# Kernel optimization log

Measured on AMD Instinct MI355X. Metric: run time of the kernel, lower is better.

## Reference

```python
import jax, jax.numpy as jnp
import numpy as np
import math

EMBED_DIM = 1024
NUM_HEADS = 16
HEAD_DIM = EMBED_DIM // NUM_HEADS
SEQ = 1024
BATCH = 8


def setup_inputs() -> dict:
    key = jax.random.key(0)
    k1, k2, k3, k4, k5 = jax.random.split(key, 5)
    q = jax.random.normal(k1, (SEQ, BATCH, EMBED_DIM), dtype=jnp.float32)
    # module asserts key == query (self-attention only)
    in_proj_w = jax.random.normal(k2, (3 * EMBED_DIM, EMBED_DIM), dtype=jnp.float32) * 0.02
    in_proj_b = jax.random.normal(k3, (3 * EMBED_DIM,), dtype=jnp.float32) * 0.02
    out_proj_w = jax.random.normal(k4, (EMBED_DIM, EMBED_DIM), dtype=jnp.float32) * 0.02
    out_proj_b = jax.random.normal(k5, (EMBED_DIM,), dtype=jnp.float32) * 0.02
    return {
        "query": q,
        "key": q,
        "value": q,
        "in_proj_w": in_proj_w,
        "in_proj_b": in_proj_b,
        "out_proj_w": out_proj_w,
        "out_proj_b": out_proj_b,
    }


def reference(query, key, value, in_proj_w, in_proj_b, out_proj_w, out_proj_b):
    s, b, e = query.shape
    nh, hd = NUM_HEADS, HEAD_DIM
    norm = math.sqrt(hd)
    # fused QKV projection: [s, b, 3e]
    mixed = query @ in_proj_w.T + in_proj_b
    mixed = mixed.reshape(s, b, nh, 3 * hd)
    q, k, v = jnp.split(mixed, 3, axis=-1)  # each [s, b, nh, hd]
    # -> [b*nh, s, hd]
    q = q.reshape(s, b * nh, hd).transpose(1, 0, 2) / norm
    k = k.reshape(s, b * nh, hd).transpose(1, 0, 2)
    v = v.reshape(s, b * nh, hd).transpose(1, 0, 2)
    # full O(s^2) attention matrix, as in the original bmm/softmax/bmm
    scores = jnp.einsum('nqd,nkd->nqk', q, k)  # [b*nh, s, s]
    probs = jax.nn.softmax(scores, axis=-1)
    ctx = jnp.einsum('nqk,nkd->nqd', probs, v)  # [b*nh, s, hd]
    # [b*nh, s, hd] -> [s, b, e]
    ctx = ctx.reshape(b, nh, s, hd).transpose(2, 0, 1, 3).reshape(s, b, e)
    return ctx @ out_proj_w.T + out_proj_b
```

## Files before the change

### kernel.cpp

```cpp
#include <hip/hip_runtime.h>

typedef __bf16 bf16_t;
typedef __bf16 bf16x4 __attribute__((ext_vector_type(4)));
typedef __bf16 bf16x8 __attribute__((ext_vector_type(8)));
typedef float f32x4 __attribute__((ext_vector_type(4)));

#define MFMA16(a, b, c) __builtin_amdgcn_mfma_f32_16x16x32_bf16((a), (b), (c), 0, 0, 0)

__device__ __forceinline__ const bf16_t* tile_ptr(const bf16_t* t, int row, int kchunk) {
    return t + row * 64 + (((kchunk ^ (row & 7))) << 3);
}

__device__ __forceinline__ void stage64(const bf16_t* __restrict__ gbase, size_t gstride,
                                        bf16_t* lds_rowbase, int lane) {
    const int rr = lane >> 3, cl = lane & 7;
    const bf16_t* g = gbase + (size_t)rr * gstride + ((cl ^ rr) << 3);
    __builtin_amdgcn_global_load_lds((__attribute__((address_space(1))) const void*)g,
                                     (__attribute__((address_space(3))) void*)lds_rowbase,
                                     16, 0, 0);
}

__device__ __forceinline__ int cs_addr(int m, int n) {
    return m * 128 + ((((n >> 3) ^ ((m >> 3) & 7))) << 3) + (n & 7);
}

__global__ void __launch_bounds__(256) k_cvt(
    const float* __restrict__ q, const float* __restrict__ wi, const float* __restrict__ wo,
    bf16_t* __restrict__ qb, bf16_t* __restrict__ wib, bf16_t* __restrict__ wob)
{
    const int g = blockIdx.x * 256 + threadIdx.x;
    const float* src; bf16_t* dst; int off;
    if (g < 1048576)      { src = q;  dst = qb;  off = g; }
    else if (g < 1441792) { src = wi; dst = wib; off = g - 1048576; }
    else                  { src = wo; dst = wob; off = g - 1441792; }
    const float4* s4 = (const float4*)(src + (size_t)off * 8);
    float4 a = s4[0], b = s4[1];
    bf16x8 v;
    v[0] = (bf16_t)a.x; v[1] = (bf16_t)a.y; v[2] = (bf16_t)a.z; v[3] = (bf16_t)a.w;
    v[4] = (bf16_t)b.x; v[5] = (bf16_t)b.y; v[6] = (bf16_t)b.z; v[7] = (bf16_t)b.w;
    *(bf16x8*)(dst + (size_t)off * 8) = v;
}

__global__ void __launch_bounds__(256) k_qkv(
    const bf16_t* __restrict__ A, const bf16_t* __restrict__ W,
    const float* __restrict__ bias,
    bf16_t* __restrict__ Qh, bf16_t* __restrict__ Kh, bf16_t* __restrict__ Vt)
{
    __shared__ bf16_t smem[16384];
    bf16_t* As = smem;
    bf16_t* Bs = smem + 8192;
    const int m0 = blockIdx.x * 128;
    const int n0 = blockIdx.y * 128;
    const int which = n0 >> 10;
    const int hbase = (n0 & 1023) >> 6;
    const int t = threadIdx.x;
    const int wave = t >> 6, lane = t & 63;
    const int quad = lane >> 4, l16 = lane & 15;
    const int wm = (wave & 1) * 64, wn = (wave >> 1) * 64;

    f32x4 acc[4][4] = {};

    for (int k0 = 0; k0 < 1024; k0 += 64) {
        __syncthreads();
        #pragma unroll
        for (int p = 0; p < 4; ++p) {
            const int rb = wave * 32 + p * 8;
            stage64(A + (size_t)(m0 + rb) * 1024 + k0, 1024, As + rb * 64, lane);
            const int np = n0 + rb;
            const int wrow = ((np & 1023) >> 6) * 192 + which * 64 + (np & 63);
            stage64(W + (size_t)wrow * 1024 + k0, 1024, Bs + rb * 64, lane);
        }
        __syncthreads();
        #pragma unroll
        for (int ks = 0; ks < 2; ++ks) {
            bf16x8 af[4], bf[4];
            #pragma unroll
            for (int i = 0; i < 4; ++i)
                af[i] = *(const bf16x8*)tile_ptr(As, wm + i * 16 + l16, ks * 4 + quad);
            #pragma unroll
            for (int j = 0; j < 4; ++j)
                bf[j] = *(const bf16x8*)tile_ptr(Bs, wn + j * 16 + l16, ks * 4 + quad);
            #pragma unroll
            for (int i = 0; i < 4; ++i)
                #pragma unroll
                for (int j = 0; j < 4; ++j)
                    acc[i][j] = MFMA16(af[i], bf[j], acc[i][j]);
        }
    }

    __syncthreads();
    const float scale = (which == 0) ? 0.180336880111112f : 1.0f;
    #pragma unroll
    for (int j = 0; j < 4; ++j) {
        const int nl = wn + j * 16 + l16;
        const float bv = bias[(hbase + (nl >> 6)) * 192 + which * 64 + (nl & 63)];
        #pragma unroll
        for (int i = 0; i < 4; ++i) {
            #pragma unroll
            for (int rg = 0; rg < 4; ++rg) {
                const int ml = wm + i * 16 + quad * 4 + rg;
                smem[cs_addr(ml, nl)] = (bf16_t)((acc[i][j][rg] + bv) * scale);
            }
        }
    }
    __syncthreads();

    const int si0 = m0 >> 3;
    if (which < 2) {
        bf16_t* dst = which ? Kh : Qh;
        #pragma unroll
        for (int u = 0; u < 4; ++u) {
            const int unit = wave * 4 + u;
            const int h = unit >> 3, bi = unit & 7;
            const int head = bi * 16 + hbase + h;
            #pragma unroll
            for (int pass = 0; pass < 2; ++pass) {
                const int si = pass * 8 + (lane >> 3);
                const int dc = lane & 7;
                const int ml = si * 8 + bi;
                const int nch = (h * 8 + dc) ^ (si & 7);
                bf16x8 v = *(const bf16x8*)&smem[ml * 128 + nch * 8];
                *(bf16x8*)(dst + (size_t)head * 65536 + (size_t)(si0 + si) * 64 + dc * 8) = v;
            }
        }
    } else {
        #pragma unroll
        for (int u = 0; u < 8; ++u) {
            const int unit = wave * 8 + u;
            const int h = unit >> 4, bi = (unit >> 1) & 7, c = unit & 1;
            const int head = bi * 16 + hbase + h;
            const int d = lane;
            bf16x8 v;
            #pragma unroll
            for (int e = 0; e < 8; ++e) {
                const int ml = (c * 8 + e) * 8 + bi;
                const int nch = (h * 8 + (d >> 3)) ^ e;
                v[e] = smem[ml * 128 + nch * 8 + (d & 7)];
            }
            *(bf16x8*)(Vt + (size_t)head * 65536 +
                       (size_t)(si0 / 8 + c) * 512 + (size_t)d * 8) = v;
        }
    }
}

__global__ void __launch_bounds__(256, 4) k_attn(
    const bf16_t* __restrict__ Qh, const bf16_t* __restrict__ Kh,
    const bf16_t* __restrict__ Vg, bf16_t* __restrict__ Ctx)
{
    __shared__ bf16_t Ks[64 * 64];
    __shared__ bf16_t Vts[64 * 64];
    __shared__ bf16_t Pw[4][32 * 64];

    const int bid = blockIdx.x;
    const int head = (bid & 7) * 16 + ((bid >> 3) & 15);
    const int qt = bid >> 7;
    const int t = threadIdx.x;
    const int wave = t >> 6, lane = t & 63;
    const int quad = lane >> 4, l16 = lane & 15;

    const bf16_t* Qg = Qh + (size_t)head * 65536 + (size_t)qt * 8192;
    const bf16_t* Kg = Kh + (size_t)head * 65536;
    const bf16_t* Vgh = Vg + (size_t)head * 65536;

    bf16x8 qf[2][2];
    #pragma unroll
    for (int half = 0; half < 2; ++half)
        #pragma unroll
        for (int ks = 0; ks < 2; ++ks)
            qf[half][ks] = *(const bf16x8*)(
                Qg + (size_t)(wave * 32 + half * 16 + l16) * 64 + ks * 32 + quad * 8);

    bf16x8 ones;
    #pragma unroll
    for (int e = 0; e < 8; ++e) ones[e] = (bf16_t)((l16 == 0) ? 1.0f : 0.0f);

    f32x4 vacc[2][5] = {};

    for (int kt = 0; kt < 16; ++kt) {
        __syncthreads();
        #pragma unroll
        for (int p = 0; p < 2; ++p) {
            const int rb = wave * 16 + p * 8;
            stage64(Kg + (size_t)(kt * 64 + rb) * 64, 64, Ks + rb * 64, lane);
            {
                const int rr = lane >> 3, cl = lane & 7;
                const bf16_t* g = Vgh + (size_t)(kt * 8 + (cl ^ rr)) * 512
                                      + (size_t)(rb + rr) * 8;
                __builtin_amdgcn_global_load_lds(
                    (__attribute__((address_space(1))) const void*)g,
                    (__attribute__((address_space(3))) void*)(Vts + rb * 64), 16, 0, 0);
            }
        }
        __syncthreads();

        f32x4 s[2][4] = {};
        #pragma unroll
        for (int ks = 0; ks < 2; ++ks) {
            #pragma unroll
            for (int j = 0; j < 4; ++j) {
                bf16x8 kf = *(const bf16x8*)tile_ptr(Ks, j * 16 + l16, ks * 4 + quad);
                s[0][j] = MFMA16(kf, qf[0][ks], s[0][j]);
                s[1][j] = MFMA16(kf, qf[1][ks], s[1][j]);
            }
        }

        #pragma unroll
        for (int half = 0; half < 2; ++half) {
            const int row = half * 16 + l16;
            #pragma unroll
            for (int j = 0; j < 4; ++j) {
                bf16x4 pv;
                #pragma unroll
                for (int rg = 0; rg < 4; ++rg)
                    pv[rg] = (bf16_t)exp2f(s[half][j][rg]);
                const int chunk = j * 2 + (quad >> 1);
                *(bf16x4*)&Pw[wave][row * 64 + ((chunk ^ (row & 7)) << 3) + (quad & 1) * 4] = pv;
            }
        }
        asm volatile("s_waitcnt lgkmcnt(0)" ::: "memory");

        #pragma unroll
        for (int ks = 0; ks < 2; ++ks) {
            bf16x8 pf0 = *(const bf16x8*)tile_ptr(Pw[wave], l16, ks * 4 + quad);
            bf16x8 pf1 = *(const bf16x8*)tile_ptr(Pw[wave], 16 + l16, ks * 4 + quad);
            #pragma unroll
            for (int n = 0; n < 4; ++n) {
                bf16x8 vf = *(const bf16x8*)tile_ptr(Vts, n * 16 + l16, ks * 4 + quad);
                vacc[0][n] = MFMA16(pf0, vf, vacc[0][n]);
                vacc[1][n] = MFMA16(pf1, vf, vacc[1][n]);
            }
            vacc[0][4] = MFMA16(pf0, ones, vacc[0][4]);
            vacc[1][4] = MFMA16(pf1, ones, vacc[1][4]);
        }
    }

    const int bi = head >> 4, h = head & 15;
    #pragma unroll
    for (int half = 0; half < 2; ++half) {
        #pragma unroll
        for (int rg = 0; rg < 4; ++rg) {
            const float l = __shfl(vacc[half][4][rg], lane & 48, 64);
            const float inv = 1.0f / l;
            const int si = qt * 128 + wave * 32 + half * 16 + quad * 4 + rg;
            #pragma unroll
            for (int n = 0; n < 4; ++n)
                Ctx[((size_t)si * 8 + bi) * 1024 + h * 64 + n * 16 + l16] =
                    (bf16_t)(vacc[half][n][rg] * inv);
        }
    }
}

__global__ void __launch_bounds__(256) k_out(
    const bf16_t* __restrict__ A, const bf16_t* __restrict__ W,
    const float* __restrict__ bias, float* __restrict__ out)
{
    __shared__ bf16_t As[128 * 64];
    __shared__ bf16_t Bs[128 * 64];
    const int m0 = blockIdx.x * 128;
    const int n0 = blockIdx.y * 128;
    const int t = threadIdx.x;
    const int wave = t >> 6, lane = t & 63;
    const int quad = lane >> 4, l16 = lane & 15;
    const int wm = (wave & 1) * 64, wn = (wave >> 1) * 64;

    f32x4 acc[4][4] = {};

    for (int k0 = 0; k0 < 1024; k0 += 64) {
        __syncthreads();
        #pragma unroll
        for (int p = 0; p < 4; ++p) {
            const int rb = wave * 32 + p * 8;
            stage64(A + (size_t)(m0 + rb) * 1024 + k0, 1024, As + rb * 64, lane);
            stage64(W + (size_t)(n0 + rb) * 1024 + k0, 1024, Bs + rb * 64, lane);
        }
        __syncthreads();
        #pragma unroll
        for (int ks = 0; ks < 2; ++ks) {
            bf16x8 af[4], bf[4];
            #pragma unroll
            for (int i = 0; i < 4; ++i)
                af[i] = *(const bf16x8*)tile_ptr(As, wm + i * 16 + l16, ks * 4 + quad);
            #pragma unroll
            for (int j = 0; j < 4; ++j)
                bf[j] = *(const bf16x8*)tile_ptr(Bs, wn + j * 16 + l16, ks * 4 + quad);
            #pragma unroll
            for (int i = 0; i < 4; ++i)
                #pragma unroll
                for (int j = 0; j < 4; ++j)
                    acc[i][j] = MFMA16(af[i], bf[j], acc[i][j]);
        }
    }

    #pragma unroll
    for (int j = 0; j < 4; ++j) {
        const int n = n0 + wn + j * 16 + l16;
        const float bv = bias[n];
        #pragma unroll
        for (int i = 0; i < 4; ++i) {
            #pragma unroll
            for (int rg = 0; rg < 4; ++rg) {
                const int m = m0 + wm + i * 16 + quad * 4 + rg;
                out[(size_t)m * 1024 + n] = acc[i][j][rg] + bv;
            }
        }
    }
}

extern "C" void kernel_launch(void* const* d_in, const int* in_sizes, int n_in,
                              void* d_out, int out_size, void* d_ws, size_t ws_size,
                              hipStream_t stream)
{
    const float* query = (const float*)d_in[0];
    const float* in_w  = (const float*)d_in[3];
    const float* in_b  = (const float*)d_in[4];
    const float* out_w = (const float*)d_in[5];
    const float* out_b = (const float*)d_in[6];
    float* out = (float*)d_out;

    bf16_t* Wi  = (bf16_t*)d_ws;
    bf16_t* Wo  = Wi + (size_t)3145728;
    bf16_t* Qh  = Wo + (size_t)1048576;
    bf16_t* Kh  = Qh + (size_t)8388608;
    bf16_t* Vt  = Kh + (size_t)8388608;
    bf16_t* Aq  = Vt + (size_t)8388608;
    bf16_t* Ctx = Aq;

    k_cvt<<<dim3(6144), 256, 0, stream>>>(query, in_w, out_w, Aq, Wi, Wo);
    k_qkv<<<dim3(64, 24), 256, 0, stream>>>(Aq, Wi, in_b, Qh, Kh, Vt);
    k_attn<<<dim3(1024), 256, 0, stream>>>(Qh, Kh, Vt, Ctx);
    k_out<<<dim3(64, 8), 256, 0, stream>>>(Ctx, Wo, out_b, out);
}
```

Baseline: 275.1 us.

## Rewrite QKV GEMM with 256x256 tiles, double-buffered LDS and interleaved MFMA

The QKV projection kernel moves from 128x128 tiles with 4 waves to 256x256 tiles with 8 waves, using 128 KB of double-buffered LDS. Global-to-LDS loads for the next k-tile are issued in pieces between MFMA groups, with explicit barriers, waitcnts and setprio around the math. A block-index swizzle remaps the 1D grid for cache locality. The goal is to hide global load latency and raise arithmetic intensity per block, at the cost of large LDS use that limits residency and of relying on hand-placed barriers for correctness.

```diff
diff --git a/kernel.cpp b/kernel.cpp
--- a/kernel.cpp
+++ b/kernel.cpp
@@ -18,10 +18,6 @@
     __builtin_amdgcn_global_load_lds((__attribute__((address_space(1))) const void*)g,
                                      (__attribute__((address_space(3))) void*)lds_rowbase,
                                      16, 0, 0);
-}
-
-__device__ __forceinline__ int cs_addr(int m, int n) {
-    return m * 128 + ((((n >> 3) ^ ((m >> 3) & 7))) << 3) + (n & 7);
 }
 
 __global__ void __launch_bounds__(256) k_cvt(
@@ -41,65 +37,100 @@
     *(bf16x8*)(dst + (size_t)off * 8) = v;
 }
 
-__global__ void __launch_bounds__(256) k_qkv(
+__global__ void __launch_bounds__(512, 2) k_qkv(
     const bf16_t* __restrict__ A, const bf16_t* __restrict__ W,
     const float* __restrict__ bias,
     bf16_t* __restrict__ Qh, bf16_t* __restrict__ Kh, bf16_t* __restrict__ Vt)
 {
-    __shared__ bf16_t smem[16384];
-    bf16_t* As = smem;
-    bf16_t* Bs = smem + 8192;
-    const int m0 = blockIdx.x * 128;
-    const int n0 = blockIdx.y * 128;
+    __shared__ bf16_t smem[65536];
+    bf16_t* const As0 = smem;
+    bf16_t* const Bs0 = smem + 16384;
+    bf16_t* const As1 = smem + 32768;
+    bf16_t* const Bs1 = smem + 49152;
+
+    const int bid = blockIdx.x;
+    const int swz = (bid & 7) * 48 + (bid >> 3);
+    const int mblk = swz / 12, nblk = swz - mblk * 12;
+    const int m0 = mblk * 256;
+    const int n0 = nblk * 256;
     const int which = n0 >> 10;
-    const int hbase = (n0 & 1023) >> 6;
+    const int hb0 = (n0 & 1023) >> 6;
     const int t = threadIdx.x;
-    const int wave = t >> 6, lane = t & 63;
+    const int wid = t >> 6, lane = t & 63;
     const int quad = lane >> 4, l16 = lane & 15;
-    const int wm = (wave & 1) * 64, wn = (wave >> 1) * 64;
-
-    f32x4 acc[4][4] = {};
-
-    for (int k0 = 0; k0 < 1024; k0 += 64) {
-        __syncthreads();
-        #pragma unroll
-        for (int p = 0; p < 4; ++p) {
-            const int rb = wave * 32 + p * 8;
-            stage64(A + (size_t)(m0 + rb) * 1024 + k0, 1024, As + rb * 64, lane);
-            const int np = n0 + rb;
-            const int wrow = ((np & 1023) >> 6) * 192 + which * 64 + (np & 63);
-            stage64(W + (size_t)wrow * 1024 + k0, 1024, Bs + rb * 64, lane);
-        }
-        __syncthreads();
-        #pragma unroll
-        for (int ks = 0; ks < 2; ++ks) {
-            bf16x8 af[4], bf[4];
-            #pragma unroll
-            for (int i = 0; i < 4; ++i)
-                af[i] = *(const bf16x8*)tile_ptr(As, wm + i * 16 + l16, ks * 4 + quad);
-            #pragma unroll
-            for (int j = 0; j < 4; ++j)
-                bf[j] = *(const bf16x8*)tile_ptr(Bs, wn + j * 16 + l16, ks * 4 + quad);
-            #pragma unroll
-            for (int i = 0; i < 4; ++i)
-                #pragma unroll
-                for (int j = 0; j < 4; ++j)
-                    acc[i][j] = MFMA16(af[i], bf[j], acc[i][j]);
-        }
-    }
-
-    __syncthreads();
-    const float scale = (which == 0) ? 0.180336880111112f : 1.0f;
+    const int wm = (wid >> 2) * 128, wn = (wid & 3) * 64;
+
+    f32x4 acc[8][4] = {};
+
+    auto stA = [&](bf16_t* dst, int kt, int p) {
+        const int rb = wid * 32 + p * 8;
+        stage64(A + (size_t)(m0 + rb) * 1024 + kt * 64, 1024, dst + rb * 64, lane);
+    };
+    auto stB = [&](bf16_t* dst, int kt, int p) {
+        const int rb = wid * 32 + p * 8;
+        const int np = n0 + rb;
+        const int wrow = ((np & 1023) >> 6) * 192 + which * 64 + (np & 63);
+        stage64(W + (size_t)wrow * 1024 + kt * 64, 1024, dst + rb * 64, lane);
+    };
+
+#define FENCE()    asm volatile("" ::: "memory")
+#define BAR()      do { FENCE(); __builtin_amdgcn_s_barrier(); FENCE(); } while (0)
+#define WAIT_LDS() asm volatile("s_waitcnt lgkmcnt(0)" ::: "memory")
+#define WAIT_VM()  asm volatile("s_waitcnt vmcnt(0)" ::: "memory")
+
+    auto ktile = [&](const bf16_t* Ac, const bf16_t* Bc, bf16_t* SA, bf16_t* SB,
+                     int skt, bool do_st) {
+        bf16x8 af[8], b0, b1;
+#define LOAD_AF(KS) { _Pragma("unroll") for (int i = 0; i < 8; ++i) \
+            af[i] = *(const bf16x8*)tile_ptr(Ac, wm + i * 16 + l16, (KS) * 4 + quad); }
+#define LOAD_B(J0, KS) { \
+            b0 = *(const bf16x8*)tile_ptr(Bc, wn + (J0) * 16 + l16, (KS) * 4 + quad); \
+            b1 = *(const bf16x8*)tile_ptr(Bc, wn + (J0) * 16 + 16 + l16, (KS) * 4 + quad); }
+#define MM16(J0) { __builtin_amdgcn_s_setprio(1); \
+            _Pragma("unroll") for (int i = 0; i < 8; ++i) { \
+                acc[i][J0] = MFMA16(af[i], b0, acc[i][J0]); \
+                acc[i][(J0) + 1] = MFMA16(af[i], b1, acc[i][(J0) + 1]); } \
+            __builtin_amdgcn_s_setprio(0); }
+
+        if (do_st) { stA(SA, skt, 0); stB(SB, skt, 0); stA(SA, skt, 1); stB(SB, skt, 1); }
+        LOAD_AF(0); LOAD_B(0, 0);
+        BAR(); WAIT_LDS(); MM16(0); BAR();
+        if (do_st) { stA(SA, skt, 2); stB(SB, skt, 2); stA(SA, skt, 3); stB(SB, skt, 3); }
+        LOAD_B(2, 0);
+        BAR(); WAIT_LDS(); MM16(2); BAR();
+        LOAD_AF(1); LOAD_B(0, 1);
+        BAR(); WAIT_LDS(); MM16(0); BAR();
+        LOAD_B(2, 1);
+        BAR(); WAIT_LDS(); MM16(2);
+#undef LOAD_AF
+#undef LOAD_B
+#undef MM16
+    };
+
+    #pragma unroll
+    for (int p = 0; p < 4; ++p) { stA(As0, 0, p); stB(Bs0, 0, p); }
+    WAIT_VM(); BAR();
+
+    #pragma unroll 1
+    for (int it = 0; it < 8; ++it) {
+        ktile(As0, Bs0, As1, Bs1, 2 * it + 1, true);
+        WAIT_VM(); BAR();
+        ktile(As1, Bs1, As0, Bs0, 2 * it + 2, it < 7);
+        WAIT_VM(); BAR();
+    }
+
+    const float scalev = (which == 0) ? 0.180336880111112f : 1.0f;
     #pragma unroll
     for (int j = 0; j < 4; ++j) {
         const int nl = wn + j * 16 + l16;
-        const float bv = bias[(hbase + (nl >> 6)) * 192 + which * 64 + (nl & 63)];
-        #pragma unroll
-        for (int i = 0; i < 4; ++i) {
+        const float bv = bias[(hb0 + (nl >> 6)) * 192 + which * 64 + (nl & 63)];
+        #pragma unroll
+        for (int i = 0; i < 8; ++i) {
             #pragma unroll
             for (int rg = 0; rg < 4; ++rg) {
                 const int ml = wm + i * 16 + quad * 4 + rg;
-                smem[cs_addr(ml, nl)] = (bf16_t)((acc[i][j][rg] + bv) * scale);
+                smem[ml * 256 + (((nl >> 3) ^ ((ml >> 3) & 7)) << 3) + (nl & 7)] =
+                    (bf16_t)((acc[i][j][rg] + bv) * scalev);
             }
         }
     }
@@ -110,37 +141,41 @@
         bf16_t* dst = which ? Kh : Qh;
         #pragma unroll
         for (int u = 0; u < 4; ++u) {
-            const int unit = wave * 4 + u;
+            const int unit = wid * 4 + u;
             const int h = unit >> 3, bi = unit & 7;
-            const int head = bi * 16 + hbase + h;
-            #pragma unroll
-            for (int pass = 0; pass < 2; ++pass) {
+            const int head = bi * 16 + hb0 + h;
+            #pragma unroll
+            for (int pass = 0; pass < 4; ++pass) {
                 const int si = pass * 8 + (lane >> 3);
                 const int dc = lane & 7;
                 const int ml = si * 8 + bi;
                 const int nch = (h * 8 + dc) ^ (si & 7);
-                bf16x8 v = *(const bf16x8*)&smem[ml * 128 + nch * 8];
+                bf16x8 v = *(const bf16x8*)&smem[ml * 256 + nch * 8];
                 *(bf16x8*)(dst + (size_t)head * 65536 + (size_t)(si0 + si) * 64 + dc * 8) = v;
             }
         }
     } else {
         #pragma unroll
-        for (int u = 0; u < 8; ++u) {
-            const int unit = wave * 8 + u;
-            const int h = unit >> 4, bi = (unit >> 1) & 7, c = unit & 1;
-            const int head = bi * 16 + hbase + h;
+        for (int u = 0; u < 16; ++u) {
+            const int unit = wid * 16 + u;
+            const int h = unit >> 5, bi = (unit >> 2) & 7, c = unit & 3;
+            const int head = bi * 16 + hb0 + h;
             const int d = lane;
             bf16x8 v;
             #pragma unroll
             for (int e = 0; e < 8; ++e) {
                 const int ml = (c * 8 + e) * 8 + bi;
                 const int nch = (h * 8 + (d >> 3)) ^ e;
-                v[e] = smem[ml * 128 + nch * 8 + (d & 7)];
+                v[e] = smem[ml * 256 + nch * 8 + (d & 7)];
             }
             *(bf16x8*)(Vt + (size_t)head * 65536 +
                        (size_t)(si0 / 8 + c) * 512 + (size_t)d * 8) = v;
         }
     }
+#undef FENCE
+#undef BAR
+#undef WAIT_LDS
+#undef WAIT_VM
 }
 
 __global__ void __launch_bounds__(256, 4) k_attn(
@@ -326,7 +361,7 @@
     bf16_t* Ctx = Aq;
 
     k_cvt<<<dim3(6144), 256, 0, stream>>>(query, in_w, out_w, Aq, Wi, Wo);
-    k_qkv<<<dim3(64, 24), 256, 0, stream>>>(Aq, Wi, in_b, Qh, Kh, Vt);
+    k_qkv<<<dim3(384), 512, 0, stream>>>(Aq, Wi, in_b, Qh, Kh, Vt);
     k_attn<<<dim3(1024), 256, 0, stream>>>(Qh, Kh, Vt, Ctx);
     k_out<<<dim3(64, 8), 256, 0, stream>>>(Ctx, Wo, out_b, out);
 }
```

Result: slower. 286.6 us (+4.2%).
